# Performance work log

Measured on AMD Instinct MI355X. Metric: run time of the kernel, lower is better.

The kernel has to match this reference:

```python
import jax, jax.numpy as jnp
import numpy as np

N_IN = 41024
N_OUT = 256


def setup_inputs() -> dict:
    key = jax.random.key(0)
    k1, k2, k3, k4 = jax.random.split(key, 4)
    B, K = 16384, 32
    ft_ics = jax.random.randint(k1, (B, K), 0, N_IN, dtype=jnp.int32)
    ft_vals = jax.random.uniform(k2, (B, K), dtype=jnp.float32)
    s = N_IN ** (-0.5)
    weight = jax.random.uniform(k3, (N_IN, N_OUT), dtype=jnp.float32) * (2 * s) - s
    bias = jax.random.uniform(k4, (N_OUT,), dtype=jnp.float32) * (2 * s) - s
    return {"ft_ics": ft_ics, "ft_vals": ft_vals, "weight": weight, "bias": bias}


def reference(ft_ics, ft_vals, weight, bias):
    # Sparse embedding-bag: out[b] = bias + sum_k weight[ft_ics[b,k]] * ft_vals[b,k]
    # ft_ics == -1 marks padding (the CUDA kernel breaks on -1); mask those.
    valid = ft_ics >= 0                                  # [B, K]
    safe_idx = jnp.where(valid, ft_ics, 0)               # in-range for gather
    vals = jnp.where(valid, ft_vals, 0.0)                # [B, K]
    gathered = weight[safe_idx]                          # [B, K, N_OUT]
    out = jnp.einsum("bk,bkd->bd", vals, gathered) + bias
    return out
```

## Files before the change

kernel.cpp:

```cpp
#include <hip/hip_runtime.h>


constexpr int K = 32;

typedef float f32x4 __attribute__((ext_vector_type(4)));

__global__ __launch_bounds__(256) void FeatureTransformer_45896020525219_kernel(
    const int* __restrict__ ics,
    const float* __restrict__ vals,
    const f32x4* __restrict__ w4,
    const f32x4* __restrict__ bias4,
    f32x4* __restrict__ out4,
    int B)
{
    const int lane   = threadIdx.x & 63;
    const int wave   = threadIdx.x >> 6;
    const int slice  = blockIdx.x & 7;
    const int rowblk = blockIdx.x >> 3;

    const int r  = lane >> 3;
    const int c4 = lane & 7;
    const int b  = rowblk * 32 + wave * 8 + r;
    if (b >= B) return;

    const int colbase = slice * 8 + c4;

    const int4   idx4 = ((const int4*)  (ics  + b * K))[c4];
    const float4 v4   = ((const float4*)(vals + b * K))[c4];

    f32x4 acc;
    {
        f32x4 bb = bias4[colbase];
        acc = bb;
    }

    const f32x4* wbase = w4 + colbase;

    f32x4 wva[8], wvb[8];
    float vva[8], vvb[8];

    auto issue = [&](const int c, f32x4* wvd, float* vvd) {
        #pragma unroll
        for (int u = 0; u < 8; ++u) {
            const int k   = c * 8 + u;
            const int src = (lane & 56) | (k >> 2);
            const int sel = k & 3;
            const int   jc = sel == 0 ? idx4.x : sel == 1 ? idx4.y
                           : sel == 2 ? idx4.z : idx4.w;
            const float vc = sel == 0 ? v4.x   : sel == 1 ? v4.y
                           : sel == 2 ? v4.z   : v4.w;
            const int   jj = __shfl(jc, src);
            const float vs = __shfl(vc, src);

            vvd[u] = (jj >= 0) ? vs : 0.0f;
            const unsigned j = (jj >= 0) ? (unsigned)jj : 0u;
            const f32x4* p  = wbase + (size_t)j * 64;
            asm volatile("global_load_dwordx4 %0, %1, off"
                         : "=v"(wvd[u]) : "v"(p));
        }
    };

    auto dofma = [&](const f32x4* wvd, const float* vvd) {
        #pragma unroll
        for (int u = 0; u < 8; ++u) {
            acc.x = fmaf(vvd[u], wvd[u].x, acc.x);
            acc.y = fmaf(vvd[u], wvd[u].y, acc.y);
            acc.z = fmaf(vvd[u], wvd[u].z, acc.z);
            acc.w = fmaf(vvd[u], wvd[u].w, acc.w);
        }
    };

    issue(0, wva, vva);
    issue(1, wvb, vvb);

    asm volatile("s_waitcnt vmcnt(8)" ::: "memory");
    __builtin_amdgcn_sched_barrier(0);
    dofma(wva, vva);
    issue(2, wva, vva);

    asm volatile("s_waitcnt vmcnt(8)" ::: "memory");
    __builtin_amdgcn_sched_barrier(0);
    dofma(wvb, vvb);
    issue(3, wvb, vvb);

    asm volatile("s_waitcnt vmcnt(8)" ::: "memory");
    __builtin_amdgcn_sched_barrier(0);
    dofma(wva, vva);

    asm volatile("s_waitcnt vmcnt(0)" ::: "memory");
    __builtin_amdgcn_sched_barrier(0);
    dofma(wvb, vvb);

    __builtin_nontemporal_store(acc, (f32x4*)(out4 + (size_t)b * 64 + colbase));
}

extern "C" void kernel_launch(void* const* d_in, const int* in_sizes, int n_in,
                              void* d_out, int out_size, void* d_ws, size_t ws_size,
                              hipStream_t stream) {
    const int*   ics   = (const int*)d_in[0];
    const float* vals  = (const float*)d_in[1];
    const f32x4* w4    = (const f32x4*)d_in[2];
    const f32x4* bias4 = (const f32x4*)d_in[3];
    f32x4*       out4  = (f32x4*)d_out;

    const int B = in_sizes[0] / K;
    const int blocks = ((B + 31) / 32) * 8;

    hipLaunchKernelGGL(FeatureTransformer_45896020525219_kernel,
                       dim3(blocks), dim3(256), 0, stream,
                       ics, vals, w4, bias4, out4, B);
}
```

Baseline: 121.7 us.

## Convert weight table to fp16 in workspace and gather half-precision rows

Adds a pre-pass kernel that converts the fp32 weight table into fp16 in the workspace buffer each call. The gather kernel then loads 8 halves per 16-byte load, halving gather bytes and using half as many blocks. The aim is to cut memory traffic in the random-row gather. In exchange it pays a full read of the fp32 table plus a write of the fp16 copy every call, and weight precision drops to fp16. An fp32 fallback remains for when the workspace is too small.

```diff
diff --git a/kernel.cpp b/kernel.cpp
--- a/kernel.cpp
+++ b/kernel.cpp
@@ -3,9 +3,120 @@
 
 constexpr int K = 32;
 
-typedef float f32x4 __attribute__((ext_vector_type(4)));
+typedef float    f32x4 __attribute__((ext_vector_type(4)));
+typedef _Float16 f16x8 __attribute__((ext_vector_type(8)));
+
+__global__ __launch_bounds__(256) void ft_cvt_w16(
+    const float4* __restrict__ w4, f16x8* __restrict__ w16, int n8)
+{
+    int i = blockIdx.x * 256 + threadIdx.x;
+    const int stride = gridDim.x * 256;
+    for (; i < n8; i += stride) {
+        const float4 a = w4[2 * i];
+        const float4 b = w4[2 * i + 1];
+        f16x8 h;
+        h[0] = (_Float16)a.x; h[1] = (_Float16)a.y;
+        h[2] = (_Float16)a.z; h[3] = (_Float16)a.w;
+        h[4] = (_Float16)b.x; h[5] = (_Float16)b.y;
+        h[6] = (_Float16)b.z; h[7] = (_Float16)b.w;
+        w16[i] = h;
+    }
+}
 
 __global__ __launch_bounds__(256) void FeatureTransformer_45896020525219_kernel(
+    const int* __restrict__ ics,
+    const float* __restrict__ vals,
+    const f16x8* __restrict__ w16,
+    const f32x4* __restrict__ bias4,
+    f32x4* __restrict__ out4,
+    int B)
+{
+    const int lane   = threadIdx.x & 63;
+    const int wave   = threadIdx.x >> 6;
+    const int slice  = blockIdx.x & 3;
+    const int rowblk = blockIdx.x >> 2;
+
+    const int r  = lane >> 3;
+    const int c4 = lane & 7;
+    const int b  = rowblk * 32 + wave * 8 + r;
+    if (b >= B) return;
+
+    const int wcol = slice * 8 + c4;
+    const f16x8* wbase = w16 + wcol;
+
+    const int4   idx4 = ((const int4*)  (ics  + (size_t)b * K))[c4];
+    const float4 v4   = ((const float4*)(vals + (size_t)b * K))[c4];
+
+    const int cb = slice * 16 + c4 * 2;
+    f32x4 acca = bias4[cb];
+    f32x4 accb = bias4[cb + 1];
+
+    f16x8 wva[8], wvb[8];
+    float vva[8], vvb[8];
+
+    auto issue = [&](const int c, f16x8* wvd, float* vvd) {
+        #pragma unroll
+        for (int u = 0; u < 8; ++u) {
+            const int k   = c * 8 + u;
+            const int src = (lane & 56) | (k >> 2);
+            const int sel = k & 3;
+            const int   jc = sel == 0 ? idx4.x : sel == 1 ? idx4.y
+                           : sel == 2 ? idx4.z : idx4.w;
+            const float vc = sel == 0 ? v4.x   : sel == 1 ? v4.y
+                           : sel == 2 ? v4.z   : v4.w;
+            const int   jj = __shfl(jc, src);
+            const float vs = __shfl(vc, src);
+
+            vvd[u] = (jj >= 0) ? vs : 0.0f;
+            const unsigned j = (jj >= 0) ? (unsigned)jj : 0u;
+            const f16x8* p  = wbase + (size_t)j * 32;
+            asm volatile("global_load_dwordx4 %0, %1, off"
+                         : "=v"(wvd[u]) : "v"(p));
+        }
+    };
+
+    auto dofma = [&](const f16x8* wvd, const float* vvd) {
+        #pragma unroll
+        for (int u = 0; u < 8; ++u) {
+            const float v = vvd[u];
+            acca.x = fmaf(v, (float)wvd[u][0], acca.x);
+            acca.y = fmaf(v, (float)wvd[u][1], acca.y);
+            acca.z = fmaf(v, (float)wvd[u][2], acca.z);
+            acca.w = fmaf(v, (float)wvd[u][3], acca.w);
+            accb.x = fmaf(v, (float)wvd[u][4], accb.x);
+            accb.y = fmaf(v, (float)wvd[u][5], accb.y);
+            accb.z = fmaf(v, (float)wvd[u][6], accb.z);
+            accb.w = fmaf(v, (float)wvd[u][7], accb.w);
+        }
+    };
+
+    issue(0, wva, vva);
+    issue(1, wvb, vvb);
+
+    asm volatile("s_waitcnt vmcnt(8)" ::: "memory");
+    __builtin_amdgcn_sched_barrier(0);
+    dofma(wva, vva);
+    issue(2, wva, vva);
+
+    asm volatile("s_waitcnt vmcnt(8)" ::: "memory");
+    __builtin_amdgcn_sched_barrier(0);
+    dofma(wvb, vvb);
+    issue(3, wvb, vvb);
+
+    asm volatile("s_waitcnt vmcnt(8)" ::: "memory");
+    __builtin_amdgcn_sched_barrier(0);
+    dofma(wva, vva);
+
+    asm volatile("s_waitcnt vmcnt(0)" ::: "memory");
+    __builtin_amdgcn_sched_barrier(0);
+    dofma(wvb, vvb);
+
+    f32x4* op = out4 + (size_t)b * 64 + cb;
+    __builtin_nontemporal_store(acca, op);
+    __builtin_nontemporal_store(accb, op + 1);
+}
+
+__global__ __launch_bounds__(256) void ft_gather_f32(
     const int* __restrict__ ics,
     const float* __restrict__ vals,
     const f32x4* __restrict__ w4,
@@ -24,16 +135,10 @@
     if (b >= B) return;
 
     const int colbase = slice * 8 + c4;
-
-    const int4   idx4 = ((const int4*)  (ics  + b * K))[c4];
-    const float4 v4   = ((const float4*)(vals + b * K))[c4];
-
-    f32x4 acc;
-    {
-        f32x4 bb = bias4[colbase];
-        acc = bb;
-    }
-
+    const int4   idx4 = ((const int4*)  (ics  + (size_t)b * K))[c4];
+    const float4 v4   = ((const float4*)(vals + (size_t)b * K))[c4];
+
+    f32x4 acc = bias4[colbase];
     const f32x4* wbase = w4 + colbase;
 
     f32x4 wva[8], wvb[8];
@@ -51,7 +156,6 @@
                            : sel == 2 ? v4.z   : v4.w;
             const int   jj = __shfl(jc, src);
             const float vs = __shfl(vc, src);
-
             vvd[u] = (jj >= 0) ? vs : 0.0f;
             const unsigned j = (jj >= 0) ? (unsigned)jj : 0u;
             const f32x4* p  = wbase + (size_t)j * 64;
@@ -59,7 +163,6 @@
                          : "=v"(wvd[u]) : "v"(p));
         }
     };
-
     auto dofma = [&](const f32x4* wvd, const float* vvd) {
         #pragma unroll
         for (int u = 0; u < 8; ++u) {
@@ -72,21 +175,17 @@
 
     issue(0, wva, vva);
     issue(1, wvb, vvb);
-
     asm volatile("s_waitcnt vmcnt(8)" ::: "memory");
     __builtin_amdgcn_sched_barrier(0);
     dofma(wva, vva);
     issue(2, wva, vva);
-
     asm volatile("s_waitcnt vmcnt(8)" ::: "memory");
     __builtin_amdgcn_sched_barrier(0);
     dofma(wvb, vvb);
     issue(3, wvb, vvb);
-
-    asm volatile("s_waitcnt vmcnt(8)" ::: "memory");
-    __builtin_amdgcn_sched_barrier(0);
-    dofma(wva, vva);
-
+    asm volatile("s_waitcnt vmcnt(8)" ::: "memory");
+    __builtin_amdgcn_sched_barrier(0);
+    dofma(wva, vva);
     asm volatile("s_waitcnt vmcnt(0)" ::: "memory");
     __builtin_amdgcn_sched_barrier(0);
     dofma(wvb, vvb);
@@ -99,14 +198,25 @@
                               hipStream_t stream) {
     const int*   ics   = (const int*)d_in[0];
     const float* vals  = (const float*)d_in[1];
-    const f32x4* w4    = (const f32x4*)d_in[2];
     const f32x4* bias4 = (const f32x4*)d_in[3];
     f32x4*       out4  = (f32x4*)d_out;
 
-    const int B = in_sizes[0] / K;
-    const int blocks = ((B + 31) / 32) * 8;
-
-    hipLaunchKernelGGL(FeatureTransformer_45896020525219_kernel,
-                       dim3(blocks), dim3(256), 0, stream,
-                       ics, vals, w4, bias4, out4, B);
-}
+    const int B   = in_sizes[0] / K;
+    const int nin = in_sizes[2] / 256;
+
+    const size_t need = (size_t)nin * 256 * 2;
+    if (ws_size >= need && d_ws != nullptr) {
+        const int n8 = nin * 32;
+        hipLaunchKernelGGL(ft_cvt_w16, dim3(1024), dim3(256), 0, stream,
+                           (const float4*)d_in[2], (f16x8*)d_ws, n8);
+        const int blocks = ((B + 31) / 32) * 4;
+        hipLaunchKernelGGL(FeatureTransformer_45896020525219_kernel,
+                           dim3(blocks), dim3(256), 0, stream,
+                           ics, vals, (const f16x8*)d_ws, bias4, out4, B);
+    } else {
+        const int blocks = ((B + 31) / 32) * 8;
+        hipLaunchKernelGGL(ft_gather_f32,
+                           dim3(blocks), dim3(256), 0, stream,
+                           ics, vals, (const f32x4*)d_in[2], bias4, out4, B);
+    }
+}
```

After: 122.4 us. Within noise of the previous version (+0.6%).
